# Performance work log

Hardware: AMD Instinct MI355X
Metric: run time of the kernel (lower is better)

Reference implementation:

```python
import jax, jax.numpy as jnp
import numpy as np
from jax import lax

NUM_COLS = 4
NUM_ROWS = 4
C = 16          # in_channels
K = 3           # kernel_size
B, H, Wd = 8, 128, 128
W_SCALE = 0.05  # keep activations stable through 16 chained ReLU convs


def setup_inputs() -> dict:
    key = jax.random.key(0)
    k1, k2 = jax.random.split(key, 2)
    x = jax.random.normal(k1, (B, C, H, Wd), dtype=jnp.float32)
    # one conv per grid cell: 3 input slots (left/below-prev/above), 3 output streams (right/up/down)
    W = jax.random.normal(k2, (NUM_COLS, NUM_ROWS, 3 * C, 3 * C, K, K), dtype=jnp.float32) * W_SCALE
    b = jnp.zeros((NUM_COLS, NUM_ROWS, 3 * C), dtype=jnp.float32)
    return {"input_tensor": x, "W": W, "b": b}


def _cell(w, bias, ins):
    # ins: list of 1..3 tensors [B, C, H, W]; zero-pad missing slots to 3*C channels
    if len(ins) < 3:
        pad_shape = (ins[0].shape[0], (3 - len(ins)) * C) + ins[0].shape[2:]
        ins = ins + [jnp.zeros(pad_shape, dtype=ins[0].dtype)]
    x = jnp.concatenate(ins, axis=1)  # [B, 3C, H, W]
    y = lax.conv_general_dilated(
        x, w, window_strides=(1, 1), padding="SAME",
        dimension_numbers=("NCHW", "OIHW", "NCHW"))
    y = jax.nn.relu(y + bias[None, :, None, None])
    right, up, down = jnp.split(y, 3, axis=1)  # each [B, C, H, W]
    return (right, up, down)


def reference(input_tensor, W, b):
    # Wavefront sweep: columns left->right, rows top->bottom.
    # outs[row] holds the (right, up, down) tuple of the most recently computed
    # cell in that row (previous column until overwritten this column).
    outs = [None] * NUM_ROWS
    for col in range(NUM_COLS):
        for row in range(NUM_ROWS):
            if col == 0:
                ins = [input_tensor] if row == 0 else [outs[row - 1][-1]]
            else:
                if row == 0:
                    ins = [outs[row][0], outs[row + 1][1]]
                elif row == NUM_ROWS - 1:
                    ins = [outs[row][0], outs[row - 1][-1]]
                else:
                    ins = [outs[row][0], outs[row + 1][1], outs[row - 1][-1]]
            outs[row] = _cell(W[col, row], b[col, row], ins)
    return outs[-1][0]
```

## Files before the change

### kernel.cpp

```cpp
#include <hip/hip_runtime.h>

#define HW    128
#define PW    130
#define NCELL 16
#define ABUF_PER_CELL 23040
#define ABUF_TOTAL (NCELL * ABUF_PER_CELL)
#define NSTREAMS 15
#define BORDER_PX 516
#define BORDER_TASKS (NSTREAMS * 8 * BORDER_PX * 2)
#define SLOT 5632

typedef _Float16 half8 __attribute__((ext_vector_type(8)));
typedef _Float16 half4 __attribute__((ext_vector_type(4)));
typedef float    f32x4 __attribute__((ext_vector_type(4)));

#define GLD_LDS(gp, lp) __builtin_amdgcn_global_load_lds( \
    (const __attribute__((address_space(1))) void*)(gp),  \
    (__attribute__((address_space(3))) void*)(lp), 16, 0, 0)

__global__ void prep_w_border_k(const float* __restrict__ W,
                                _Float16* __restrict__ Abuf,
                                _Float16* __restrict__ sbase) {
    int idx = blockIdx.x * 256 + threadIdx.x;
    if (idx < ABUF_TOTAL) {
        int j = idx & 7;
        int t = idx >> 3;
        int co = t % 48;   t /= 48;
        int quad = t & 3;  t >>= 2;
        int chunk = t % 5; t /= 5;
        int slot = t % 3;  t /= 3;
        int cell = t;
        int g = chunk * 4 + quad;
        float v = 0.f;
        if (g < 18) {
            int kh = g / 6, r6 = g % 6;
            int kw = r6 >> 1, cg = r6 & 1;
            int ci = slot * 16 + cg * 8 + j;
            v = W[((size_t)(cell * 48 + co) * 48 + ci) * 9 + kh * 3 + kw];
        }
        Abuf[idx] = (_Float16)v;
        return;
    }
    int t = idx - ABUF_TOTAL;
    if (t >= BORDER_TASKS) return;
    int h  = t & 1;
    int pb = t >> 1;
    int p  = pb % BORDER_PX;
    int bb = pb / BORDER_PX;
    int y, x;
    if (p < 260) {
        y = (p < 130) ? 0 : (PW - 1);
        x = p - ((p < 130) ? 0 : 130);
    } else {
        int e = p - 260;
        y = 1 + (e >> 1);
        x = (e & 1) ? (PW - 1) : 0;
    }
    half8 z = {};
    *(half8*)(sbase + (size_t)bb * (PW * PW * 16)
              + ((size_t)y * PW + x) * 16 + h * 8) = z;
}

struct CellIO {
    const _Float16* in0; const _Float16* in1; const _Float16* in2;
    const _Float16* Ac; const float* bc;
    _Float16* o0; _Float16* o1; _Float16* o2;
    float* fout;
};

template<int LIVE, int NIN, bool FIN, bool XIN>
__device__ __forceinline__ void cell_body(const CellIO& P, int b, _Float16* xh,
                                          const float* xsrc)
{
    const int tid = threadIdx.x;
    const int bx = blockIdx.x, by = blockIdx.y;
    const int x0 = bx * 16, y0 = by * 16;
    const int lane = tid & 63, wv = tid >> 6;
    const int n = lane & 15, quad = lane >> 4;
    const int py0 = wv * 4;

    float bv[3][4];
    half8 a0[3][3];

    if constexpr (XIN) {
        for (int task = tid; task < 288; task += 256) {
            int ci = task / 18, iy = task - (task / 18) * 18;
            float v[18];
#pragma unroll
            for (int ix = 0; ix < 18; ++ix) v[ix] = 0.f;
            int gy = y0 + iy - 1;
            if ((unsigned)gy < (unsigned)HW) {
                const float* rp = xsrc + (((size_t)b * 16 + ci) * HW + gy) * HW + x0;
                f32x4 q0 = *(const f32x4*)(rp);
                f32x4 q1 = *(const f32x4*)(rp + 4);
                f32x4 q2 = *(const f32x4*)(rp + 8);
                f32x4 q3 = *(const f32x4*)(rp + 12);
#pragma unroll
                for (int j = 0; j < 4; ++j) {
                    v[1 + j] = q0[j]; v[5 + j] = q1[j];
                    v[9 + j] = q2[j]; v[13 + j] = q3[j];
                }
                if (x0 > 0)       v[0]  = rp[-1];
                if (x0 < HW - 16) v[17] = rp[16];
            }
            int cg = ci >> 3, cj = ci & 7;
#pragma unroll
            for (int ix = 0; ix < 18; ++ix)
                xh[(((iy * 2 + cg) * 18) + ix) * 8 + cj] = (_Float16)v[ix];
        }
        __syncthreads();
    } else {
        const _Float16* const ins[3] = {P.in0, P.in1, P.in2};
        auto stage = [&](int s) {
            const _Float16* src = ins[s] + (size_t)b * (PW * PW * 16)
                                 + ((size_t)(by * 16) * PW + bx * 16) * 16;
            _Float16* base = xh + s * SLOT;
#pragma unroll
            for (int k = 0; k < 3; ++k) {
                int kk = wv + k * 4;
                if (kk < 11) {
                    int u = kk * 64 + lane;
                    int iy = u / 36, r36 = u - iy * 36;
                    int cg = r36 / 18, ix = r36 - cg * 18;
                    GLD_LDS(src + (iy * PW + ix) * 16 + cg * 8, base + kk * 512);
                }
            }
        };
        stage(0);
        if constexpr (NIN >= 2) {
            asm volatile("" ::: "memory");
#pragma unroll
            for (int cot = 0; cot < 3; ++cot) {
                if (!(LIVE & (1 << cot))) continue;
#pragma unroll
                for (int r = 0; r < 4; ++r) bv[cot][r] = P.bc[cot * 16 + quad * 4 + r];
            }
            const _Float16* As0 = P.Ac + quad * 384 + n * 8;
#pragma unroll
            for (int c = 0; c < 3; ++c)
#pragma unroll
                for (int cot = 0; cot < 3; ++cot) {
                    if (!(LIVE & (1 << cot))) continue;
                    a0[c][cot] = *(const half8*)(As0 + c * 1536 + cot * 128);
                }
            asm volatile("" ::: "memory");
#pragma unroll
            for (int s = 1; s < NIN; ++s) stage(s);
            if (wv == 3) asm volatile("s_waitcnt vmcnt(%0)" :: "n"((NIN - 1) * 2) : "memory");
            else         asm volatile("s_waitcnt vmcnt(%0)" :: "n"((NIN - 1) * 3) : "memory");
            __builtin_amdgcn_s_barrier();
            asm volatile("" ::: "memory");
        } else {
            __syncthreads();
        }
    }

    int base_c[5];
#pragma unroll
    for (int c = 0; c < 5; ++c) {
        int g = c * 4 + quad;
        if (g >= 18) g = 0;
        int kh = g / 6, r6 = g % 6;
        int kw = r6 >> 1, cg = r6 & 1;
        base_c[c] = ((py0 + kh) * 2 + cg) * 18 + n + kw;
    }

    constexpr bool PIPE = (!XIN) && (NIN >= 2);
    f32x4 acc[3][4];
#pragma unroll
    for (int cot = 0; cot < 3; ++cot) {
        if (!(LIVE & (1 << cot))) continue;
#pragma unroll
        for (int r = 0; r < 4; ++r) {
            float bvv = PIPE ? bv[cot][r] : P.bc[cot * 16 + quad * 4 + r];
#pragma unroll
            for (int nt = 0; nt < 4; ++nt) acc[cot][nt][r] = bvv;
        }
    }

#pragma unroll
    for (int s = 0; s < NIN; ++s) {
        if (PIPE && s == 1) __syncthreads();
        const _Float16* sxh = xh + s * SLOT;
        const _Float16* As = P.Ac + (size_t)(s * 5) * 1536 + quad * 384 + n * 8;
#pragma unroll
        for (int c = 0; c < 5; ++c) {
            half8 Bh[4];
#pragma unroll
            for (int nt = 0; nt < 4; ++nt)
                Bh[nt] = *(const half8*)(sxh + (base_c[c] + nt * 36) * 8);
            const _Float16* Ab = As + (size_t)c * 1536;
#pragma unroll
            for (int cot = 0; cot < 3; ++cot) {
                if (!(LIVE & (1 << cot))) continue;
                half8 ah;
                if constexpr (PIPE) {
                    if (s == 0 && c < 3) ah = a0[c][cot];
                    else                 ah = *(const half8*)(Ab + cot * 128);
                } else {
                    ah = *(const half8*)(Ab + cot * 128);
                }
#pragma unroll
                for (int nt = 0; nt < 4; ++nt)
                    acc[cot][nt] = __builtin_amdgcn_mfma_f32_16x16x32_f16(ah, Bh[nt], acc[cot][nt], 0, 0, 0);
            }
        }
    }

    if constexpr (FIN) {
#pragma unroll
        for (int nt = 0; nt < 4; ++nt) {
            int y = y0 + py0 + nt, xg = x0 + n;
#pragma unroll
            for (int r = 0; r < 4; ++r) {
                float vv = acc[0][nt][r];
                P.fout[(((size_t)b * 16 + quad * 4 + r) * HW + y) * HW + xg] = vv > 0.f ? vv : 0.f;
            }
        }
    } else {
        _Float16* const outs[3] = {P.o0, P.o1, P.o2};
#pragma unroll
        for (int cot = 0; cot < 3; ++cot) {
            if (!(LIVE & (1 << cot))) continue;
            _Float16* op = outs[cot] + (size_t)b * (PW * PW * 16);
#pragma unroll
            for (int nt = 0; nt < 4; ++nt) {
                int y = y0 + py0 + nt;
                half4 hv;
#pragma unroll
                for (int r = 0; r < 4; ++r) {
                    float vv = acc[cot][nt][r];
                    hv[r] = (_Float16)(vv > 0.f ? vv : 0.f);
                }
                *(half4*)(op + ((size_t)(y + 1) * PW + x0 + n + 1) * 16 + quad * 4) = hv;
            }
        }
    }
}

template<int L0, int N0, int L1, int N1, bool FIN, bool XIN>
__global__ __launch_bounds__(256, 4) void cell_k(CellIO P0, CellIO P1,
                                                 const float* xsrc) {
    constexpr int MAXN = (N0 > N1) ? N0 : N1;
    __shared__ __align__(16) _Float16 xh[MAXN * SLOT];
    int b = blockIdx.z & 7;
    if constexpr (L1 > 0) {
        if (blockIdx.z >= 8) { cell_body<L1, N1, false, false>(P1, b, xh, nullptr); return; }
    }
    cell_body<L0, N0, FIN, XIN>(P0, b, xh, xsrc);
}

extern "C" void kernel_launch(void* const* d_in, const int* in_sizes, int n_in,
                              void* d_out, int out_size, void* d_ws, size_t ws_size,
                              hipStream_t stream) {
    const float* x  = (const float*)d_in[0];
    const float* W  = (const float*)d_in[1];
    const float* bi = (const float*)d_in[2];
    float* out = (float*)d_out;

    _Float16* Abuf = (_Float16*)d_ws;
    const size_t abytes = (size_t)NCELL * ABUF_PER_CELL * 2;
    _Float16* q = (_Float16*)((char*)d_ws + abytes);
    _Float16* sbase = q;
    const size_t S = (size_t)8 * PW * PW * 16;

    _Float16 *R[2][4], *U[4], *D[2][2];
    for (int pa = 0; pa < 2; ++pa)
        for (int r = 0; r < 4; ++r) { R[pa][r] = q; q += S; }
    U[0] = nullptr;
    for (int r = 1; r < 4; ++r) { U[r] = q; q += S; }
    D[0][0] = q; q += S; D[0][1] = q; q += S;
    D[1][0] = q; q += S; D[1][1] = q; q += S;

    hipLaunchKernelGGL(prep_w_border_k,
                       dim3((ABUF_TOTAL + BORDER_TASKS + 255) / 256),
                       dim3(256), 0, stream, W, Abuf, sbase);

    auto mkio = [&](int c, int r) -> CellIO {
        CellIO io{};
        if (c == 0) {
            io.in0 = (r == 0) ? nullptr : D[0][(r - 1) & 1];
        } else {
            io.in0 = R[(c - 1) & 1][r];
            if (r == 0)      io.in1 = U[1];
            else if (r == 3) io.in1 = D[c & 1][0];
            else { io.in1 = U[r + 1]; io.in2 = D[c & 1][(r - 1) & 1]; }
        }
        if (c < 3) {
            io.o0 = R[c & 1][r];
            if (r > 0) io.o1 = U[r];
            if (r < 3) io.o2 = D[c & 1][r & 1];
        } else {
            if (r < 3) io.o2 = D[1][r & 1];
            else       io.fout = out;
        }
        io.Ac = Abuf + (size_t)(c * 4 + r) * ABUF_PER_CELL;
        io.bc = bi + (size_t)(c * 4 + r) * 48;
        return io;
    };

    dim3 blk(256), g1(8, 8, 8), g2(8, 8, 16);
#define ONEX(c, r)       do { CellIO a = mkio(c, r); \
    hipLaunchKernelGGL((cell_k<5, 1, 0, 0, false, true>), g1, blk, 0, stream, a, a, x); } while (0)
#define ONE(L, N, c, r)  do { CellIO a = mkio(c, r); \
    hipLaunchKernelGGL((cell_k<L, N, 0, 0, false, false>), g1, blk, 0, stream, a, a, x); } while (0)
#define ONEF(c, r)       do { CellIO a = mkio(c, r); \
    hipLaunchKernelGGL((cell_k<1, 2, 0, 0, true, false>), g1, blk, 0, stream, a, a, x); } while (0)
#define TWO(L0, N0, c0, r0, L1, N1, c1, r1) do { \
    CellIO a = mkio(c0, r0), bb2 = mkio(c1, r1); \
    hipLaunchKernelGGL((cell_k<L0, N0, L1, N1, false, false>), g2, blk, 0, stream, a, bb2, x); } while (0)

    ONEX(0, 0);
    ONE(7, 1, 0, 1);
    TWO(7, 1, 0, 2,  5, 2, 1, 0);
    TWO(3, 1, 0, 3,  7, 3, 1, 1);
    TWO(7, 3, 1, 2,  5, 2, 2, 0);
    TWO(3, 2, 1, 3,  7, 3, 2, 1);
    TWO(7, 3, 2, 2,  4, 2, 3, 0);
    TWO(3, 2, 2, 3,  4, 3, 3, 1);
    ONE(4, 3, 3, 2);
    ONEF(3, 3);
#undef ONEX
#undef ONE
#undef ONEF
#undef TWO
}
```

Baseline: 186.9 us.

## Reorder MFMA chunk schedule to overlap staged input loads and prefetch weights

Bias and the first weight fragments are now loaded for every non-XIN path before staging begins, including single-input cells. The MFMA loop is flattened into one chunk sequence. In the pipelined case it runs the first three chunks of slot 0 first, then the later input slots, then the remaining slot-0 chunks, so compute can proceed while the other slots' global-to-LDS loads complete. MFMA groups are wrapped in s_setprio to favor the matrix-issuing waves, at the cost of more register pressure from the hoisted A fragments.

Result: faster. 165.1 us (median of 2 runs) (-11.7%).

```diff
diff --git a/kernel.cpp b/kernel.cpp
--- a/kernel.cpp
+++ b/kernel.cpp
@@ -126,15 +126,13 @@
                 }
             }
         };
-        stage(0);
-        if constexpr (NIN >= 2) {
-            asm volatile("" ::: "memory");
-#pragma unroll
-            for (int cot = 0; cot < 3; ++cot) {
-                if (!(LIVE & (1 << cot))) continue;
-#pragma unroll
-                for (int r = 0; r < 4; ++r) bv[cot][r] = P.bc[cot * 16 + quad * 4 + r];
-            }
+#pragma unroll
+        for (int cot = 0; cot < 3; ++cot) {
+            if (!(LIVE & (1 << cot))) continue;
+#pragma unroll
+            for (int r = 0; r < 4; ++r) bv[cot][r] = P.bc[cot * 16 + quad * 4 + r];
+        }
+        {
             const _Float16* As0 = P.Ac + quad * 384 + n * 8;
 #pragma unroll
             for (int c = 0; c < 3; ++c)
@@ -143,6 +141,10 @@
                     if (!(LIVE & (1 << cot))) continue;
                     a0[c][cot] = *(const half8*)(As0 + c * 1536 + cot * 128);
                 }
+        }
+        asm volatile("" ::: "memory");
+        stage(0);
+        if constexpr (NIN >= 2) {
             asm volatile("" ::: "memory");
 #pragma unroll
             for (int s = 1; s < NIN; ++s) stage(s);
@@ -172,39 +174,45 @@
         if (!(LIVE & (1 << cot))) continue;
 #pragma unroll
         for (int r = 0; r < 4; ++r) {
-            float bvv = PIPE ? bv[cot][r] : P.bc[cot * 16 + quad * 4 + r];
+            float bvv = XIN ? P.bc[cot * 16 + quad * 4 + r] : bv[cot][r];
 #pragma unroll
             for (int nt = 0; nt < 4; ++nt) acc[cot][nt][r] = bvv;
         }
     }
 
-#pragma unroll
-    for (int s = 0; s < NIN; ++s) {
-        if (PIPE && s == 1) __syncthreads();
+    constexpr int NC = NIN * 5;
+#pragma unroll
+    for (int i = 0; i < NC; ++i) {
+        int s, c;
+        if constexpr (PIPE) {
+            if (i < 3)                        { s = 0; c = i; }
+            else if (i < 3 + 5 * (NIN - 1))   { s = 1 + (i - 3) / 5; c = (i - 3) % 5; }
+            else                              { s = 0; c = i - 5 * (NIN - 1); }
+        } else { s = i / 5; c = i % 5; }
+        if (PIPE && i == 3) __syncthreads();
+
         const _Float16* sxh = xh + s * SLOT;
-        const _Float16* As = P.Ac + (size_t)(s * 5) * 1536 + quad * 384 + n * 8;
-#pragma unroll
-        for (int c = 0; c < 5; ++c) {
-            half8 Bh[4];
+        half8 Bh[4];
+#pragma unroll
+        for (int nt = 0; nt < 4; ++nt)
+            Bh[nt] = *(const half8*)(sxh + (base_c[c] + nt * 36) * 8);
+        const _Float16* Ab = P.Ac + (size_t)(s * 5 + c) * 1536 + quad * 384 + n * 8;
+        half8 ah[3];
+#pragma unroll
+        for (int cot = 0; cot < 3; ++cot) {
+            if (!(LIVE & (1 << cot))) continue;
+            if (!XIN && s == 0 && c < 3) ah[cot] = a0[c][cot];
+            else                         ah[cot] = *(const half8*)(Ab + cot * 128);
+        }
+        __builtin_amdgcn_s_setprio(1);
+#pragma unroll
+        for (int cot = 0; cot < 3; ++cot) {
+            if (!(LIVE & (1 << cot))) continue;
 #pragma unroll
             for (int nt = 0; nt < 4; ++nt)
-                Bh[nt] = *(const half8*)(sxh + (base_c[c] + nt * 36) * 8);
-            const _Float16* Ab = As + (size_t)c * 1536;
-#pragma unroll
-            for (int cot = 0; cot < 3; ++cot) {
-                if (!(LIVE & (1 << cot))) continue;
-                half8 ah;
-                if constexpr (PIPE) {
-                    if (s == 0 && c < 3) ah = a0[c][cot];
-                    else                 ah = *(const half8*)(Ab + cot * 128);
-                } else {
-                    ah = *(const half8*)(Ab + cot * 128);
-                }
-#pragma unroll
-                for (int nt = 0; nt < 4; ++nt)
-                    acc[cot][nt] = __builtin_amdgcn_mfma_f32_16x16x32_f16(ah, Bh[nt], acc[cot][nt], 0, 0, 0);
-            }
-        }
+                acc[cot][nt] = __builtin_amdgcn_mfma_f32_16x16x32_f16(ah[cot], Bh[nt], acc[cot][nt], 0, 0, 0);
+        }
+        __builtin_amdgcn_s_setprio(0);
     }
 
     if constexpr (FIN) {
```
